# Performance work log

Hardware: AMD Instinct MI355X
Metric: run time of the kernel (lower is better)

The kernel has to match this reference:

```python
import jax, jax.numpy as jnp
import numpy as np

B, TV, TS, D = 16, 256, 32, 512


def setup_inputs() -> dict:
    key = jax.random.key(0)
    ks = jax.random.split(key, 8)
    return {
        "video_feature": jax.random.normal(ks[0], (B, TV, D), dtype=jnp.float32),
        "video_mask": jnp.ones((B, TV), dtype=jnp.float32),
        "sentence_feature": jax.random.normal(ks[1], (B, TS, D), dtype=jnp.float32),
        "sentence_mask": jnp.ones((B, TS), dtype=jnp.float32),
        "w1": jax.random.normal(ks[2], (D, D), dtype=jnp.float32) * (1.0 / np.sqrt(D)),
        "b1": jax.random.normal(ks[3], (D,), dtype=jnp.float32) * 0.02,
        "w2": jax.random.normal(ks[4], (D, D), dtype=jnp.float32) * (1.0 / np.sqrt(D)),
        "wt": jax.random.normal(ks[5], (D,), dtype=jnp.float32) * (1.0 / np.sqrt(D)),
    }


def reference(video_feature, video_mask, sentence_feature, sentence_mask, w1, b1, w2, wt):
    # tmp1: [B, Tv, D] masked video projection (Linear with bias)
    tmp1 = (jnp.einsum("bvd,ed->bve", video_feature, w1) + b1) * video_mask[:, :, None]
    # tmp2: [B, Ts, D] masked sentence projection (Linear, no bias)
    tmp2 = jnp.einsum("bsd,ed->bse", sentence_feature, w2) * sentence_mask[:, :, None]
    # pairwise mask: [B, Tv, Ts]
    pair_mask = video_mask[:, :, None] * sentence_mask[:, None, :]
    # broadcast-add -> [B, Tv, Ts, D], mask, tanh, reduce with wt -> [B, Tv, Ts]
    tmp = (tmp1[:, :, None, :] + tmp2[:, None, :, :]) * pair_mask[..., None]
    M = jnp.einsum("bvsd,d->bvs", jnp.tanh(tmp), wt)
    return M * pair_mask
```

## Files before the change

kernel.cpp:

```cpp
#include <hip/hip_runtime.h>

#define BB 16
#define TV 256
#define TS 32
#define DD 512

typedef float    floatx4  __attribute__((ext_vector_type(4)));
typedef float    floatx2  __attribute__((ext_vector_type(2)));
typedef short    short8   __attribute__((ext_vector_type(8)));
typedef unsigned short ushort8 __attribute__((ext_vector_type(8)));

#define TANH_SCALE 2.885390082f

static __device__ __forceinline__ unsigned short f2bf(float f) {
    unsigned int u = __float_as_uint(f);
    u += 0x7FFFu + ((u >> 16) & 1u);
    return (unsigned short)(u >> 16);
}

__global__ __launch_bounds__(256) void ta_convert(
    const float* __restrict__ video, const float* __restrict__ sent,
    const float* __restrict__ w1,    const float* __restrict__ w2,
    unsigned short* __restrict__ vb, unsigned short* __restrict__ sb,
    unsigned short* __restrict__ w1b, unsigned short* __restrict__ w2b)
{
    const int NV = BB * TV * DD, NS = BB * TS * DD, NW = DD * DD;
    const int base = (blockIdx.x * 256 + threadIdx.x) * 8;
    const float* src; unsigned short* dst; int off;
    if      (base < NV)           { src = video; dst = vb;  off = base; }
    else if (base < NV + NS)      { src = sent;  dst = sb;  off = base - NV; }
    else if (base < NV + NS + NW) { src = w1;    dst = w1b; off = base - NV - NS; }
    else                          { src = w2;    dst = w2b; off = base - NV - NS - NW; }
    const float4 a = *(const float4*)(src + off);
    const float4 b = *(const float4*)(src + off + 4);
    ushort8 o;
    o[0] = f2bf(a.x); o[1] = f2bf(a.y); o[2] = f2bf(a.z); o[3] = f2bf(a.w);
    o[4] = f2bf(b.x); o[5] = f2bf(b.y); o[6] = f2bf(b.z); o[7] = f2bf(b.w);
    *(ushort8*)(dst + off) = o;
}

__global__ __launch_bounds__(256) void ta_mfma_gemm(
    const unsigned short* __restrict__ vb, const unsigned short* __restrict__ w1b,
    const float* __restrict__ b1,          const float* __restrict__ vmask,
    float* __restrict__ tmp1,
    const unsigned short* __restrict__ sb, const unsigned short* __restrict__ w2b,
    const float* __restrict__ smask,       unsigned short* __restrict__ tmp2,
    const float* __restrict__ wt,          float* __restrict__ wsum)
{
    const int t = threadIdx.x;

    if (blockIdx.x == 0 && t < 64) {
        float v = 0.f;
        for (int i = t; i < DD; i += 64) v += wt[i];
        for (int off = 32; off; off >>= 1) v += __shfl_down(v, off);
        if (t == 0) wsum[0] = v;
    }

    const bool g2 = (blockIdx.x >= 512);
    const int bid = g2 ? (int)blockIdx.x - 512 : (int)blockIdx.x;
    const unsigned short* __restrict__ A = g2 ? sb    : vb;
    const unsigned short* __restrict__ W = g2 ? w2b   : w1b;
    const float* __restrict__ rm         = g2 ? smask : vmask;
    const int m0 = (g2 ? (bid & 7)  : (bid & 63)) * 64;
    const int n0 = (g2 ? (bid >> 3) : (bid >> 6)) * 64;

    __shared__ unsigned short As[2][4096];
    __shared__ unsigned short Bs[2][4096];

    const int lane = t & 63;
    const int wid  = t >> 6;
    const int wm   = wid >> 1, wn = wid & 1;
    const int lr   = lane & 15, kg = lane >> 4;

    const int r0 = t >> 3,          g0c = (t & 7) ^ (r0 & 7);
    const int r1 = (t + 256) >> 3,  g1c = (t & 7) ^ (r1 & 7);
    const unsigned short* a0p = A + (size_t)(m0 + r0) * DD + g0c * 8;
    const unsigned short* a1p = A + (size_t)(m0 + r1) * DD + g1c * 8;
    const unsigned short* w0p = W + (size_t)(n0 + r0) * DD + g0c * 8;
    const unsigned short* w1p = W + (size_t)(n0 + r1) * DD + g1c * 8;
    const int l0 = t * 8;
    const int l1 = (t + 256) * 8;

#define TA_STAGE(buf, koff) do {                                               \
    __builtin_amdgcn_global_load_lds(                                          \
        (const __attribute__((address_space(1))) void*)(a0p + (koff)),         \
        (__attribute__((address_space(3))) void*)&As[buf][l0], 16, 0, 0);      \
    __builtin_amdgcn_global_load_lds(                                          \
        (const __attribute__((address_space(1))) void*)(a1p + (koff)),         \
        (__attribute__((address_space(3))) void*)&As[buf][l1], 16, 0, 0);      \
    __builtin_amdgcn_global_load_lds(                                          \
        (const __attribute__((address_space(1))) void*)(w0p + (koff)),         \
        (__attribute__((address_space(3))) void*)&Bs[buf][l0], 16, 0, 0);      \
    __builtin_amdgcn_global_load_lds(                                          \
        (const __attribute__((address_space(1))) void*)(w1p + (koff)),         \
        (__attribute__((address_space(3))) void*)&Bs[buf][l1], 16, 0, 0);      \
  } while (0)

    floatx4 acc[2][2] = {};

    const int ml0 = wm * 32 + lr, ml1 = ml0 + 16;
    const int nl0 = wn * 32 + lr, nl1 = nl0 + 16;
    const int sa0 = ml0 * 64, sa1 = ml1 * 64;
    const int sb0 = nl0 * 64, sb1 = nl1 * 64;
    const int xa = ml0 & 7, xb = nl0 & 7;

    TA_STAGE(0, 0);
    __syncthreads();

    int cur = 0;
    for (int step = 0; step < 8; ++step) {
        if (step < 7) TA_STAGE(cur ^ 1, (step + 1) * 64);
#pragma unroll
        for (int kk = 0; kk < 2; ++kk) {
            const int kc = kk * 4 + kg;
            short8 a0 = *(const short8*)&As[cur][sa0 + ((kc ^ xa) << 3)];
            short8 a1 = *(const short8*)&As[cur][sa1 + ((kc ^ xa) << 3)];
            short8 b0 = *(const short8*)&Bs[cur][sb0 + ((kc ^ xb) << 3)];
            short8 b1 = *(const short8*)&Bs[cur][sb1 + ((kc ^ xb) << 3)];
            acc[0][0] = __builtin_amdgcn_mfma_f32_16x16x32_bf16(a0, b0, acc[0][0], 0, 0, 0);
            acc[0][1] = __builtin_amdgcn_mfma_f32_16x16x32_bf16(a0, b1, acc[0][1], 0, 0, 0);
            acc[1][0] = __builtin_amdgcn_mfma_f32_16x16x32_bf16(a1, b0, acc[1][0], 0, 0, 0);
            acc[1][1] = __builtin_amdgcn_mfma_f32_16x16x32_bf16(a1, b1, acc[1][1], 0, 0, 0);
        }
        __syncthreads();
        cur ^= 1;
    }
#undef TA_STAGE

#pragma unroll
    for (int fm = 0; fm < 2; ++fm)
#pragma unroll
        for (int fn = 0; fn < 2; ++fn)
#pragma unroll
            for (int r = 0; r < 4; ++r) {
                const int m = m0 + wm * 32 + fm * 16 + kg * 4 + r;
                const int n = n0 + wn * 32 + fn * 16 + lr;
                const float mk = rm[m] * TANH_SCALE;
                const float val = acc[fm][fn][r];
                if (!g2) tmp1[(size_t)m * DD + n] = (val + b1[n]) * mk;
                else     tmp2[(size_t)m * DD + n] = f2bf(val * mk);
            }
}

__global__ __launch_bounds__(512) void ta_tanh_main(
    const float* __restrict__ tmp1,
    const unsigned short* __restrict__ tmp2,
    const float* __restrict__ wt,
    const float* __restrict__ wsum,
    const float* __restrict__ vmask,
    const float* __restrict__ smask,
    float* __restrict__ out)
{
    __shared__ unsigned short t2s[TS * DD];
    __shared__ float part[512];

    const int t  = threadIdx.x;
    const int b  = blockIdx.x >> 6;
    const int v0 = (blockIdx.x & 63) << 2;

    {
        const unsigned short* src = tmp2 + (size_t)b * TS * DD;
#pragma unroll
        for (int i = 0; i < 4; ++i) {
            const int chunk = t + 512 * i;
            const int row = chunk >> 6;
            const int c   = chunk & 63;
            ushort8 val = *(const ushort8*)&src[chunk * 8];
            *(ushort8*)&t2s[row * DD + ((c ^ (row & 15)) << 3)] = val;
        }
    }
    __syncthreads();

    const int s  = t & 31;
    const int vi = (t >> 5) & 3;
    const int q  = __builtin_amdgcn_readfirstlane(t >> 7);
    const int v  = v0 + vi;

    const float pm = vmask[b * TV + v] * smask[b * TS + s];
    const float* __restrict__ x1p = tmp1 + ((size_t)(b * TV + v)) * DD + q * 128;
    const float* __restrict__ wtp = wt + q * 128;
    const int rowbase = s * DD;
    const int swz = s & 15;

    floatx4 acc4a = {0.f, 0.f, 0.f, 0.f};
    floatx4 acc4b = {0.f, 0.f, 0.f, 0.f};
#pragma unroll 2
    for (int i = 0; i < 16; ++i) {
        uint4 u4 = *(const uint4*)&t2s[rowbase + (((q * 16 + i) ^ swz) << 3)];
        floatx4 x1a = *(const floatx4*)(x1p + i * 8);
        floatx4 x1b = *(const floatx4*)(x1p + i * 8 + 4);
        floatx4 wa  = *(const floatx4*)(wtp + i * 8);
        floatx4 wb  = *(const floatx4*)(wtp + i * 8 + 4);
        floatx4 x2a = { __uint_as_float(u4.x << 16), __uint_as_float(u4.x & 0xffff0000u),
                        __uint_as_float(u4.y << 16), __uint_as_float(u4.y & 0xffff0000u) };
        floatx4 x2b = { __uint_as_float(u4.z << 16), __uint_as_float(u4.z & 0xffff0000u),
                        __uint_as_float(u4.w << 16), __uint_as_float(u4.w & 0xffff0000u) };
        floatx4 za = x1a + x2a;
        floatx4 zb = x1b + x2b;
        floatx4 ea = { __builtin_amdgcn_exp2f(za[0]), __builtin_amdgcn_exp2f(za[1]),
                       __builtin_amdgcn_exp2f(za[2]), __builtin_amdgcn_exp2f(za[3]) };
        floatx4 eb = { __builtin_amdgcn_exp2f(zb[0]), __builtin_amdgcn_exp2f(zb[1]),
                       __builtin_amdgcn_exp2f(zb[2]), __builtin_amdgcn_exp2f(zb[3]) };
        ea = ea + 1.f;
        eb = eb + 1.f;
        floatx4 ra = { __builtin_amdgcn_rcpf(ea[0]), __builtin_amdgcn_rcpf(ea[1]),
                       __builtin_amdgcn_rcpf(ea[2]), __builtin_amdgcn_rcpf(ea[3]) };
        floatx4 rb = { __builtin_amdgcn_rcpf(eb[0]), __builtin_amdgcn_rcpf(eb[1]),
                       __builtin_amdgcn_rcpf(eb[2]), __builtin_amdgcn_rcpf(eb[3]) };
        acc4a = acc4a + wa * ra;
        acc4b = acc4b + wb * rb;
    }

    part[t] = (acc4a[0] + acc4a[1]) + (acc4a[2] + acc4a[3])
            + (acc4b[0] + acc4b[1]) + (acc4b[2] + acc4b[3]);
    __syncthreads();

    if (t < 128) {
        const float sum = part[t] + part[t + 128] + part[t + 256] + part[t + 384];
        const int s2 = t & 31, vi2 = t >> 5;
        const int v2 = v0 + vi2;
        const float pm2 = vmask[b * TV + v2] * smask[b * TS + s2];
        out[((size_t)b * TV + v2) * TS + s2] = pm2 * (wsum[0] - 2.f * sum);
    }
}

extern "C" void kernel_launch(void* const* d_in, const int* in_sizes, int n_in,
                              void* d_out, int out_size, void* d_ws, size_t ws_size,
                              hipStream_t stream)
{
    const float* video = (const float*)d_in[0];
    const float* vmask = (const float*)d_in[1];
    const float* sent  = (const float*)d_in[2];
    const float* smask = (const float*)d_in[3];
    const float* w1    = (const float*)d_in[4];
    const float* b1    = (const float*)d_in[5];
    const float* w2    = (const float*)d_in[6];
    const float* wt    = (const float*)d_in[7];
    float* out = (float*)d_out;

    const size_t NV = (size_t)BB * TV * DD, NS = (size_t)BB * TS * DD, NW = (size_t)DD * DD;

    float* tmp1          = (float*)d_ws;
    unsigned short* tmp2 = (unsigned short*)(tmp1 + NV);
    unsigned short* vb   = tmp2 + NS;
    unsigned short* sb   = vb + NV;
    unsigned short* w1b  = sb + NS;
    unsigned short* w2b  = w1b + NW;
    float* wsum          = (float*)(w2b + NW);

    const int total8 = (int)((NV + NS + 2 * NW) / 8);
    ta_convert<<<dim3(total8 / 256), dim3(256), 0, stream>>>(
        video, sent, w1, w2, vb, sb, w1b, w2b);
    ta_mfma_gemm<<<dim3(512 + 64), dim3(256), 0, stream>>>(
        vb, w1b, b1, vmask, tmp1, sb, w2b, smask, tmp2, wt, wsum);
    ta_tanh_main<<<dim3(BB * (TV / 4)), dim3(512), 0, stream>>>(
        tmp1, tmp2, wt, wsum, vmask, smask, out);
}
```

Before: 40.51 us.

## Factor exp2 of sum into product of precomputed exponentials in GEMM epilogue

Uses exp2(a+b)=exp2(a)*exp2(b): the GEMM epilogue now stores exp2 of the scaled projections, so the O(B*Tv*Ts*D) inner loop does a multiply-add and a reciprocal instead of an add, exp2, add and reciprocal. tmp2 is stored as transposed fp32 (d-major, s-minor) for conflict-free LDS reads, and the four tmp1 rows are staged in shared memory. This doubles the LDS footprint for tmp2 and raises its traffic, and overflow/underflow of the separate exponentials can change accuracy for large activations.

```diff
diff --git a/kernel.cpp b/kernel.cpp
--- a/kernel.cpp
+++ b/kernel.cpp
@@ -6,7 +6,6 @@
 #define DD 512
 
 typedef float    floatx4  __attribute__((ext_vector_type(4)));
-typedef float    floatx2  __attribute__((ext_vector_type(2)));
 typedef short    short8   __attribute__((ext_vector_type(8)));
 typedef unsigned short ushort8 __attribute__((ext_vector_type(8)));
 
@@ -42,9 +41,9 @@
 __global__ __launch_bounds__(256) void ta_mfma_gemm(
     const unsigned short* __restrict__ vb, const unsigned short* __restrict__ w1b,
     const float* __restrict__ b1,          const float* __restrict__ vmask,
-    float* __restrict__ tmp1,
+    float* __restrict__ tmp1e,
     const unsigned short* __restrict__ sb, const unsigned short* __restrict__ w2b,
-    const float* __restrict__ smask,       unsigned short* __restrict__ tmp2,
+    const float* __restrict__ smask,       float* __restrict__ tmp2e,
     const float* __restrict__ wt,          float* __restrict__ wsum)
 {
     const int t = threadIdx.x;
@@ -137,21 +136,27 @@
                 const int n = n0 + wn * 32 + fn * 16 + lr;
                 const float mk = rm[m] * TANH_SCALE;
                 const float val = acc[fm][fn][r];
-                if (!g2) tmp1[(size_t)m * DD + n] = (val + b1[n]) * mk;
-                else     tmp2[(size_t)m * DD + n] = f2bf(val * mk);
+                if (!g2) {
+                    tmp1e[(size_t)m * DD + n] =
+                        __builtin_amdgcn_exp2f((val + b1[n]) * mk);
+                } else {
+                    tmp2e[(size_t)(m >> 5) * DD * TS + (size_t)n * TS + (m & 31)] =
+                        __builtin_amdgcn_exp2f(val * mk);
+                }
             }
 }
 
 __global__ __launch_bounds__(512) void ta_tanh_main(
-    const float* __restrict__ tmp1,
-    const unsigned short* __restrict__ tmp2,
+    const float* __restrict__ tmp1e,
+    const float* __restrict__ tmp2e,
     const float* __restrict__ wt,
     const float* __restrict__ wsum,
     const float* __restrict__ vmask,
     const float* __restrict__ smask,
     float* __restrict__ out)
 {
-    __shared__ unsigned short t2s[TS * DD];
+    __shared__ float t2s[DD * TS];
+    __shared__ float e1s[4 * DD];
     __shared__ float part[512];
 
     const int t  = threadIdx.x;
@@ -159,54 +164,45 @@
     const int v0 = (blockIdx.x & 63) << 2;
 
     {
-        const unsigned short* src = tmp2 + (size_t)b * TS * DD;
-#pragma unroll
-        for (int i = 0; i < 4; ++i) {
-            const int chunk = t + 512 * i;
-            const int row = chunk >> 6;
-            const int c   = chunk & 63;
-            ushort8 val = *(const ushort8*)&src[chunk * 8];
-            *(ushort8*)&t2s[row * DD + ((c ^ (row & 15)) << 3)] = val;
-        }
+        const float4* src = (const float4*)(tmp2e + (size_t)b * DD * TS);
+        float4* dst = (float4*)t2s;
+#pragma unroll
+        for (int i = 0; i < 8; ++i) dst[t + 512 * i] = src[t + 512 * i];
+        const int c = t * 4, row = c >> 9, col = c & 511;
+        *(float4*)&e1s[c] =
+            *(const float4*)&tmp1e[(size_t)(b * TV + v0 + row) * DD + col];
     }
     __syncthreads();
 
     const int s  = t & 31;
     const int vi = (t >> 5) & 3;
     const int q  = __builtin_amdgcn_readfirstlane(t >> 7);
-    const int v  = v0 + vi;
-
-    const float pm = vmask[b * TV + v] * smask[b * TS + s];
-    const float* __restrict__ x1p = tmp1 + ((size_t)(b * TV + v)) * DD + q * 128;
+
+    const float* __restrict__ e1p = e1s + vi * DD + q * 128;
     const float* __restrict__ wtp = wt + q * 128;
-    const int rowbase = s * DD;
-    const int swz = s & 15;
+    const int tbase = q * 4096 + s;
 
     floatx4 acc4a = {0.f, 0.f, 0.f, 0.f};
     floatx4 acc4b = {0.f, 0.f, 0.f, 0.f};
 #pragma unroll 2
     for (int i = 0; i < 16; ++i) {
-        uint4 u4 = *(const uint4*)&t2s[rowbase + (((q * 16 + i) ^ swz) << 3)];
-        floatx4 x1a = *(const floatx4*)(x1p + i * 8);
-        floatx4 x1b = *(const floatx4*)(x1p + i * 8 + 4);
+        floatx4 e1a = *(const floatx4*)(e1p + i * 8);
+        floatx4 e1b = *(const floatx4*)(e1p + i * 8 + 4);
         floatx4 wa  = *(const floatx4*)(wtp + i * 8);
         floatx4 wb  = *(const floatx4*)(wtp + i * 8 + 4);
-        floatx4 x2a = { __uint_as_float(u4.x << 16), __uint_as_float(u4.x & 0xffff0000u),
-                        __uint_as_float(u4.y << 16), __uint_as_float(u4.y & 0xffff0000u) };
-        floatx4 x2b = { __uint_as_float(u4.z << 16), __uint_as_float(u4.z & 0xffff0000u),
-                        __uint_as_float(u4.w << 16), __uint_as_float(u4.w & 0xffff0000u) };
-        floatx4 za = x1a + x2a;
-        floatx4 zb = x1b + x2b;
-        floatx4 ea = { __builtin_amdgcn_exp2f(za[0]), __builtin_amdgcn_exp2f(za[1]),
-                       __builtin_amdgcn_exp2f(za[2]), __builtin_amdgcn_exp2f(za[3]) };
-        floatx4 eb = { __builtin_amdgcn_exp2f(zb[0]), __builtin_amdgcn_exp2f(zb[1]),
-                       __builtin_amdgcn_exp2f(zb[2]), __builtin_amdgcn_exp2f(zb[3]) };
-        ea = ea + 1.f;
-        eb = eb + 1.f;
-        floatx4 ra = { __builtin_amdgcn_rcpf(ea[0]), __builtin_amdgcn_rcpf(ea[1]),
-                       __builtin_amdgcn_rcpf(ea[2]), __builtin_amdgcn_rcpf(ea[3]) };
-        floatx4 rb = { __builtin_amdgcn_rcpf(eb[0]), __builtin_amdgcn_rcpf(eb[1]),
-                       __builtin_amdgcn_rcpf(eb[2]), __builtin_amdgcn_rcpf(eb[3]) };
+        const int dof = tbase + i * 256;
+        float e20 = t2s[dof];        float e21 = t2s[dof + 32];
+        float e22 = t2s[dof + 64];   float e23 = t2s[dof + 96];
+        float e24 = t2s[dof + 128];  float e25 = t2s[dof + 160];
+        float e26 = t2s[dof + 192];  float e27 = t2s[dof + 224];
+        floatx4 da = { e1a[0] * e20 + 1.f, e1a[1] * e21 + 1.f,
+                       e1a[2] * e22 + 1.f, e1a[3] * e23 + 1.f };
+        floatx4 db = { e1b[0] * e24 + 1.f, e1b[1] * e25 + 1.f,
+                       e1b[2] * e26 + 1.f, e1b[3] * e27 + 1.f };
+        floatx4 ra = { __builtin_amdgcn_rcpf(da[0]), __builtin_amdgcn_rcpf(da[1]),
+                       __builtin_amdgcn_rcpf(da[2]), __builtin_amdgcn_rcpf(da[3]) };
+        floatx4 rb = { __builtin_amdgcn_rcpf(db[0]), __builtin_amdgcn_rcpf(db[1]),
+                       __builtin_amdgcn_rcpf(db[2]), __builtin_amdgcn_rcpf(db[3]) };
         acc4a = acc4a + wa * ra;
         acc4b = acc4b + wb * rb;
     }
@@ -240,9 +236,9 @@
 
     const size_t NV = (size_t)BB * TV * DD, NS = (size_t)BB * TS * DD, NW = (size_t)DD * DD;
 
-    float* tmp1          = (float*)d_ws;
-    unsigned short* tmp2 = (unsigned short*)(tmp1 + NV);
-    unsigned short* vb   = tmp2 + NS;
+    float* tmp1e         = (float*)d_ws;
+    float* tmp2e         = tmp1e + NV;
+    unsigned short* vb   = (unsigned short*)(tmp2e + NS);
     unsigned short* sb   = vb + NV;
     unsigned short* w1b  = sb + NS;
     unsigned short* w2b  = w1b + NW;
@@ -252,7 +248,7 @@
     ta_convert<<<dim3(total8 / 256), dim3(256), 0, stream>>>(
         video, sent, w1, w2, vb, sb, w1b, w2b);
     ta_mfma_gemm<<<dim3(512 + 64), dim3(256), 0, stream>>>(
-        vb, w1b, b1, vmask, tmp1, sb, w2b, smask, tmp2, wt, wsum);
+        vb, w1b, b1, vmask, tmp1e, sb, w2b, smask, tmp2e, wt, wsum);
     ta_tanh_main<<<dim3(BB * (TV / 4)), dim3(512), 0, stream>>>(
-        tmp1, tmp2, wt, wsum, vmask, smask, out);
-}
+        tmp1e, tmp2e, wt, wsum, vmask, smask, out);
+}
```

Measured after the change: 37.05 us. 1.09x faster.
